# Kernel optimization log

Hardware: AMD Instinct MI355X
Metric: run time of the kernel (lower is better)

Reference implementation:

```python
import jax, jax.numpy as jnp
import numpy as np

B, T, D, H = 8, 1024, 512, 8
HD = D // H  # head_dim = 64


def conv1d(x, w, b):
    # x: [B, C_in, T], w: [C_out, C_in, 3], 'same' padding
    y = jax.lax.conv_general_dilated(x, w, (1,), [(1, 1)],
                                     dimension_numbers=('NCH', 'OIH', 'NCH'))
    return y + b[None, :, None]


def setup_inputs() -> dict:
    key = jax.random.key(0)
    ks = jax.random.split(key, 9)
    s = 0.05
    return {
        'x': jax.random.normal(ks[0], (B, T, D), dtype=jnp.float32),
        'w11': jax.random.normal(ks[1], (D, D, 3), dtype=jnp.float32) * s,
        'b11': jnp.zeros((D,), dtype=jnp.float32),
        'w12': jax.random.normal(ks[2], (D, D, 3), dtype=jnp.float32) * s,
        'b12': jnp.zeros((D,), dtype=jnp.float32),
        'w13': jax.random.normal(ks[3], (D, D, 3), dtype=jnp.float32) * s,
        'b13': jnp.zeros((D,), dtype=jnp.float32),
        'w2': jax.random.normal(ks[4], (D, 2 * D, 3), dtype=jnp.float32) * s,
        'b2': jnp.zeros((D,), dtype=jnp.float32),
    }


def reference(x, w11, b11, w12, b12, w13, b13, w2, b2):
    # dropout is identity in eval mode
    b, t, d = x.shape
    xc = jnp.transpose(x, (0, 2, 1))  # [B, D, T]

    def proj(w, bb):
        y = jax.nn.relu(conv1d(xc, w, bb))        # [B, D, T]
        y = jnp.transpose(y, (0, 2, 1))           # [B, T, D]
        return y.reshape(b, t, H, HD)             # [B, T, H, HD]

    q = proj(w11, b11)
    k = proj(w12, b12)
    v = proj(w13, b13)

    # ---- time-wise attention (d_k = head_dim) ----
    qf = jnp.transpose(q, (0, 2, 1, 3))  # [B, H, T, HD]
    kf = jnp.transpose(k, (0, 2, 1, 3))
    vf = jnp.transpose(v, (0, 2, 1, 3))
    sf = jnp.einsum('bhtd,bhsd->bhts', qf, kf) / np.sqrt(HD)  # [B,H,T,T]
    af = jax.nn.softmax(sf, axis=-1)
    valuesf = jnp.einsum('bhts,bhsd->bhtd', af, vf)           # [B,H,T,HD]
    valuesf = jnp.transpose(valuesf, (0, 2, 1, 3)).reshape(b, t, H * HD)

    # ---- channel-wise attention (d_k = T, scores over head_dim) ----
    qt = jnp.transpose(q, (0, 2, 3, 1))  # [B, H, HD, T]
    kt = jnp.transpose(k, (0, 2, 3, 1))
    vt = jnp.transpose(v, (0, 2, 3, 1))
    st = jnp.einsum('bhct,bhdt->bhcd', qt, kt) / np.sqrt(t)   # [B,H,HD,HD]
    at = jax.nn.softmax(st, axis=-1)
    valuest = jnp.einsum('bhcd,bhdt->bhct', at, vt)           # [B,H,HD,T]
    # torch: permute(0,2,3,1).reshape(B, T, H*HD)
    valuest = jnp.transpose(valuest, (0, 2, 3, 1)).reshape(b, t, H * HD)

    values = jnp.concatenate([valuesf, valuest], axis=-1)     # [B, T, 2D]
    values = jnp.transpose(values, (0, 2, 1))                 # [B, 2D, T]
    out = jax.nn.relu(conv1d(values, w2, b2))                 # [B, D, T]
    return jnp.transpose(out, (0, 2, 1))                      # [B, T, D]
```

## Files before the change

### kernel.cpp

```cpp
#include <hip/hip_runtime.h>

#define BB 8
#define TT 1024
#define DD 512
#define DD2 1024
#define HH 8
#define HDIM 64
#define TP (TT + 2)

typedef short short8 __attribute__((ext_vector_type(8)));
typedef float floatx4 __attribute__((ext_vector_type(4)));

typedef const __attribute__((address_space(1))) unsigned int* gas_ptr;
typedef __attribute__((address_space(3))) unsigned int* las_ptr;

__device__ __forceinline__ unsigned short f2bf(float f) {
    union { float f; unsigned u; } v; v.f = f;
    unsigned r = v.u + 0x7fffu + ((v.u >> 16) & 1u);
    return (unsigned short)(r >> 16);
}

__device__ __forceinline__ void gl2lds16(const void* g, void* l) {
    __builtin_amdgcn_global_load_lds((gas_ptr)g, (las_ptr)l, 16, 0, 0);
}

#define NX4BLK 4104
#define NW1BLK 9216
#define NW2BLK 6144
#define NZBLK 1024
__global__ void k_prep(const float* __restrict__ x, const float* __restrict__ w0,
                       const float* __restrict__ w1, const float* __restrict__ w2,
                       const float* __restrict__ wo,
                       unsigned short* __restrict__ xp, unsigned short* __restrict__ wqkv,
                       unsigned short* __restrict__ w2k, unsigned short* __restrict__ vp,
                       float* __restrict__ gbuf) {
    int blk = blockIdx.x;
    if (blk < NX4BLK) {
        int idx = blk * 256 + threadIdx.x;
        int c4 = idx % (DD / 4);
        int rt = idx / (DD / 4);
        int row = rt % TP;
        int b = rt / TP;
        ushort4 o = {0, 0, 0, 0};
        if (row >= 1 && row <= TT) {
            float4 vv = *(const float4*)&x[((size_t)(b * TT + row - 1)) * DD + c4 * 4];
            o.x = f2bf(vv.x); o.y = f2bf(vv.y); o.z = f2bf(vv.z); o.w = f2bf(vv.w);
        }
        *(ushort4*)&xp[(size_t)idx * 4] = o;
        return;
    }
    blk -= NX4BLK;
    if (blk < NW1BLK) {
        int idx = blk * 256 + threadIdx.x;
        int e = idx & 7;
        int lane = (idx >> 3) & 63;
        int co0 = (idx >> 9) & 31;
        int ci0 = (idx >> 14) & 15;
        int rest = idx >> 18;
        int k = rest % 3, p = rest / 3;
        int co = co0 * 16 + (lane & 15);
        int ci = ci0 * 32 + (lane >> 4) * 8 + e;
        const float* w = (p == 0) ? w0 : ((p == 1) ? w1 : w2);
        wqkv[idx] = f2bf(w[(co * DD + ci) * 3 + k]);
        return;
    }
    blk -= NW1BLK;
    if (blk < NW2BLK) {
        int idx = blk * 256 + threadIdx.x;
        int e = idx & 7;
        int lane = (idx >> 3) & 63;
        int co0 = (idx >> 9) & 31;
        int ci0 = (idx >> 14) & 31;
        int k = idx >> 19;
        int co = co0 * 16 + (lane & 15);
        int ci = ci0 * 32 + (lane >> 4) * 8 + e;
        w2k[idx] = f2bf(wo[(co * DD2 + ci) * 3 + k]);
        return;
    }
    blk -= NW2BLK;
    {
        int idx = blk * 256 + threadIdx.x;
        if (idx < BB * 2 * 2 * DD) {
            int c = idx % (2 * DD);
            int t1 = idx / (2 * DD);
            int row = (t1 & 1) ? (TT + 1) : 0;
            int b = t1 >> 1;
            vp[(b * TP + row) * (2 * DD) + c] = 0;
        }
        if (idx < 64 * HDIM * HDIM) gbuf[idx] = 0.f;
    }
}

__global__ __launch_bounds__(256) void k_qkv_conv(
    const unsigned short* __restrict__ xp, const unsigned short* __restrict__ wfrag,
    const float* __restrict__ b11, const float* __restrict__ b12, const float* __restrict__ b13,
    unsigned short* __restrict__ q, unsigned short* __restrict__ qt,
    unsigned short* __restrict__ kfrag, unsigned short* __restrict__ kt,
    unsigned short* __restrict__ v, unsigned short* __restrict__ vtfrag) {
    __shared__ short As[2][80 * 64];
    int wave = threadIdx.x >> 6, lane = threadIdx.x & 63;
    int l15 = lane & 15, quad = lane >> 4;
    int tb = blockIdx.x * 64;
    int cb = blockIdx.y * 128;
    int proj = blockIdx.z % 3, b = blockIdx.z / 3;
    const short* A = (const short*)xp + b * TP * DD;
    const short* WF = (const short*)wfrag + (size_t)proj * 786432 + lane * 8;
    int srow8 = lane >> 3;
    int scl = ((lane & 7) ^ srow8) * 8;
    int co0b = (cb >> 4) + wave * 2;

    floatx4 acc[4][2];
#pragma unroll
    for (int mi = 0; mi < 4; ++mi)
#pragma unroll
        for (int ni = 0; ni < 2; ++ni) acc[mi][ni] = (floatx4){0.f, 0.f, 0.f, 0.f};

    auto stage = [&](int it) {
        short* dst = As[it & 1];
        int cib = it * 64;
        for (int g = wave; g < 10; g += 4) {
            int j = g >> 1, hf = g & 1;
            int row = hf * 8 + srow8;
            gl2lds16(A + (tb + j * 16 + row) * DD + cib + scl, &dst[j * 1024 + hf * 512]);
        }
    };

    stage(0);
    __syncthreads();

    for (int it = 0; it < 8; ++it) {
        if (it < 7) stage(it + 1);
        const short* Asb = As[it & 1];
#pragma unroll
        for (int k = 0; k < 3; ++k) {
            short8 bf[2][2];
#pragma unroll
            for (int kf = 0; kf < 2; ++kf)
#pragma unroll
                for (int ni = 0; ni < 2; ++ni)
                    bf[kf][ni] = *(const short8*)(WF +
                        ((size_t)((k * 16 + it * 2 + kf) * 32 + co0b + ni) << 9));
#pragma unroll
            for (int kf = 0; kf < 2; ++kf) {
                short8 af[4];
#pragma unroll
                for (int mi = 0; mi < 4; ++mi) {
                    int arow = mi * 16 + l15 + k;
                    int cl = kf * 4 + quad;
                    af[mi] = *(const short8*)&Asb[arow * 64 + ((cl ^ (arow & 7)) << 3)];
                }
#pragma unroll
                for (int mi = 0; mi < 4; ++mi)
#pragma unroll
                    for (int ni = 0; ni < 2; ++ni)
                        acc[mi][ni] = __builtin_amdgcn_mfma_f32_16x16x32_bf16(af[mi], bf[kf][ni], acc[mi][ni], 0, 0, 0);
            }
        }
        __syncthreads();
    }

    const float* bias = (proj == 0) ? b11 : ((proj == 1) ? b12 : b13);
#pragma unroll
    for (int ni = 0; ni < 2; ++ni) {
        int co = cb + wave * 32 + ni * 16 + l15;
        float bv = bias[co];
        int h = co >> 6, hd = co & 63;
        int bh = b * HH + h;
#pragma unroll
        for (int mi = 0; mi < 4; ++mi) {
            int tbase = tb + mi * 16 + quad * 4;
            unsigned short bb[4];
            ushort4 pk;
#pragma unroll
            for (int r = 0; r < 4; ++r) {
                float val = fmaxf(acc[mi][ni][r] + bv, 0.f);
                bb[r] = f2bf(val);
                ((unsigned short*)&pk)[r] = bb[r];
            }
            if (proj == 0) {
#pragma unroll
                for (int r = 0; r < 4; ++r)
                    q[((size_t)bh * TT + tbase + r) * HDIM + hd] = bb[r];
                *(ushort4*)&qt[((size_t)bh * HDIM + hd) * TT + tbase] = pk;
            } else if (proj == 1) {
                *(ushort4*)&kt[((size_t)bh * HDIM + hd) * TT + tbase] = pk;
                int sblk = tbase >> 6;
                int jr = (quad & 1) + 2 * (mi >> 1);
                int l15a_base = 4 * (quad >> 1) + 8 * (mi & 1);
                int kf = hd >> 5, quad_a = (hd >> 3) & 3, elem = hd & 7;
                size_t base = ((((size_t)bh * 16 + sblk) * 4 + jr) * 2 + kf) * 512 +
                              quad_a * 128 + elem;
#pragma unroll
                for (int r = 0; r < 4; ++r)
                    kfrag[base + (l15a_base + r) * 8] = bb[r];
            } else {
#pragma unroll
                for (int r = 0; r < 4; ++r)
                    v[((size_t)bh * TT + tbase + r) * HDIM + hd] = bb[r];
                int sblk = tbase >> 6;
                int df = hd >> 4, l15a = hd & 15;
                int kf = mi >> 1;
                int quad_a = 2 * (mi & 1) + (quad >> 1);
                int elem = (quad & 1) * 4;
                size_t base = ((((size_t)bh * 16 + sblk) * 4 + df) * 2 + kf) * 512 +
                              (quad_a * 16 + l15a) * 8 + elem;
                *(ushort4*)&vtfrag[base] = pk;
            }
        }
    }
}

__global__ __launch_bounds__(256) void k_attn_gram(
    const unsigned short* __restrict__ q, const unsigned short* __restrict__ kfrag,
    const unsigned short* __restrict__ vtfrag, const unsigned short* __restrict__ qt,
    const unsigned short* __restrict__ kt, float* __restrict__ gbuf,
    unsigned short* __restrict__ vp) {
    __shared__ short kvs[2][8192];
    int wave = threadIdx.x >> 6, lane = threadIdx.x & 63;
    int l15 = lane & 15, quad = lane >> 4;
    int bh = blockIdx.y;

    if (blockIdx.x < 16) {
        int b = bh >> 3, h = bh & 7;
        int qr = blockIdx.x * 64 + wave * 16;
        const short* Q = (const short*)q + (size_t)bh * TT * HDIM;
        const short* KF = (const short*)kfrag + (size_t)bh * 16 * 8 * 512 + lane * 8;
        const short* VF = (const short*)vtfrag + (size_t)bh * 16 * 8 * 512 + lane * 8;

        short8 bq[2];
#pragma unroll
        for (int kf = 0; kf < 2; ++kf)
            bq[kf] = *(const short8*)(Q + (qr + l15) * HDIM + kf * 32 + quad * 8);

        floatx4 o[4];
#pragma unroll
        for (int df = 0; df < 4; ++df) o[df] = (floatx4){0.f, 0.f, 0.f, 0.f};
        float lacc = 0.f;

        auto stagekv = [&](int s) {
            short* dst = kvs[s & 1];
            for (int f = wave; f < 8; f += 4) {
                gl2lds16(KF + s * 4096 + f * 512, &dst[f * 512]);
                gl2lds16(VF + s * 4096 + f * 512, &dst[4096 + f * 512]);
            }
        };

        stagekv(0);
        __syncthreads();

        for (int sblk = 0; sblk < 16; ++sblk) {
            if (sblk < 15) stagekv(sblk + 1);
            const short* kb = (const short*)&kvs[sblk & 1][0] + lane * 8;
            const short* vb = kb + 4096;
            floatx4 c[4];
#pragma unroll
            for (int jr = 0; jr < 4; ++jr) c[jr] = (floatx4){0.f, 0.f, 0.f, 0.f};
#pragma unroll
            for (int jr = 0; jr < 4; ++jr) {
#pragma unroll
                for (int kf = 0; kf < 2; ++kf) {
                    short8 ak = *(const short8*)(kb + (jr * 2 + kf) * 512);
                    c[jr] = __builtin_amdgcn_mfma_f32_16x16x32_bf16(ak, bq[kf], c[jr], 0, 0, 0);
                }
            }
            short8 pb[2];
#pragma unroll
            for (int kf = 0; kf < 2; ++kf) {
                union { short8 s; unsigned u[4]; } pk;
#pragma unroll
                for (int half = 0; half < 2; ++half) {
                    floatx4 cc = c[2 * kf + half];
                    float p0 = __expf(cc[0] * 0.125f);
                    float p1 = __expf(cc[1] * 0.125f);
                    float p2 = __expf(cc[2] * 0.125f);
                    float p3 = __expf(cc[3] * 0.125f);
                    lacc += (p0 + p1) + (p2 + p3);
                    pk.u[half * 2] =
                        __builtin_amdgcn_perm(__float_as_uint(p1), __float_as_uint(p0), 0x07060302u);
                    pk.u[half * 2 + 1] =
                        __builtin_amdgcn_perm(__float_as_uint(p3), __float_as_uint(p2), 0x07060302u);
                }
                pb[kf] = pk.s;
            }
#pragma unroll
            for (int df = 0; df < 4; ++df) {
#pragma unroll
                for (int kf = 0; kf < 2; ++kf) {
                    short8 av = *(const short8*)(vb + (df * 2 + kf) * 512);
                    o[df] = __builtin_amdgcn_mfma_f32_16x16x32_bf16(av, pb[kf], o[df], 0, 0, 0);
                }
            }
            __syncthreads();
        }

        lacc += __shfl_xor(lacc, 16);
        lacc += __shfl_xor(lacc, 32);
        float linv = 1.f / lacc;

        unsigned short* vrow = vp + (size_t)(b * TP + 1 + qr + l15) * (2 * DD) + h * 64;
#pragma unroll
        for (int df = 0; df < 4; ++df) {
            ushort4 pk;
#pragma unroll
            for (int r = 0; r < 4; ++r) ((unsigned short*)&pk)[r] = f2bf(o[df][r] * linv);
            *(ushort4*)&vrow[df * 16 + quad * 4] = pk;
        }
    } else {
        int tc = blockIdx.x - 16;
        const short* Qt = (const short*)qt + (size_t)bh * HDIM * TT;
        const short* Kt = (const short*)kt + (size_t)bh * HDIM * TT;

        floatx4 g[4];
#pragma unroll
        for (int nt = 0; nt < 4; ++nt) g[nt] = (floatx4){0.f, 0.f, 0.f, 0.f};

        int t0b = tc * 256;
        for (int t0 = 0; t0 < 256; t0 += 32) {
            short8 aq = *(const short8*)(Qt + (wave * 16 + l15) * TT + t0b + t0 + quad * 8);
#pragma unroll
            for (int nt = 0; nt < 4; ++nt) {
                short8 bk = *(const short8*)(Kt + (nt * 16 + l15) * TT + t0b + t0 + quad * 8);
                g[nt] = __builtin_amdgcn_mfma_f32_16x16x32_bf16(aq, bk, g[nt], 0, 0, 0);
            }
        }
        float* gb = gbuf + bh * HDIM * HDIM;
#pragma unroll
        for (int nt = 0; nt < 4; ++nt) {
#pragma unroll
            for (int r = 0; r < 4; ++r) {
                int row = wave * 16 + quad * 4 + r;
                atomicAdd(&gb[row * HDIM + nt * 16 + l15], g[nt][r]);
            }
        }
    }
}

__global__ __launch_bounds__(256) void k_chan_av(
    const float* __restrict__ gbuf, const unsigned short* __restrict__ v,
    unsigned short* __restrict__ vp) {
    __shared__ short lds_a[64 * 64];
    int wave = threadIdx.x >> 6, lane = threadIdx.x & 63;
    int l15 = lane & 15, quad = lane >> 4;
    int tc = blockIdx.x, bh = blockIdx.y;
    int b = bh >> 3, h = bh & 7;
    const float sc = 0.03125f;

    if (threadIdx.x < 64) {
        const float* gb = gbuf + bh * HDIM * HDIM + threadIdx.x * HDIM;
        float mx = -3.0e38f;
        for (int j = 0; j < 64; ++j) mx = fmaxf(mx, gb[j] * sc);
        float sum = 0.f;
        for (int j = 0; j < 64; ++j) sum += __expf(gb[j] * sc - mx);
        float inv = 1.f / sum;
        for (int j = 0; j < 64; ++j)
            lds_a[threadIdx.x * 64 + j] = (short)f2bf(__expf(gb[j] * sc - mx) * inv);
    }
    __syncthreads();

    const short* V = (const short*)v + (size_t)bh * TT * HDIM;
    short8 pa[2];
#pragma unroll
    for (int kf = 0; kf < 2; ++kf)
        pa[kf] = *(const short8*)&lds_a[(wave * 16 + l15) * 64 + kf * 32 + quad * 8];

    for (int tt = 0; tt < 16; ++tt) {
        int ttile = tc * 16 + tt;
        floatx4 c = (floatx4){0.f, 0.f, 0.f, 0.f};
#pragma unroll
        for (int kf = 0; kf < 2; ++kf) {
            short8 bv = *(const short8*)(V + (ttile * 16 + l15) * HDIM + kf * 32 + quad * 8);
            c = __builtin_amdgcn_mfma_f32_16x16x32_bf16(pa[kf], bv, c, 0, 0, 0);
        }
        int t = ttile * 16 + l15;
#pragma unroll
        for (int r = 0; r < 4; ++r) {
            int crow = wave * 16 + quad * 4 + r;
            int tout = crow * 16 + (t >> 6);
            int col = 512 + ((t & 63) << 3) + h;
            vp[(b * TP + 1 + tout) * (2 * DD) + col] = f2bf(c[r]);
        }
    }
}

__global__ __launch_bounds__(256) void k_out_conv(
    const unsigned short* __restrict__ vp, const unsigned short* __restrict__ w2k,
    const float* __restrict__ b2, float* __restrict__ out) {
    __shared__ short As[2][144 * 64];
    int wave = threadIdx.x >> 6, lane = threadIdx.x & 63;
    int l15 = lane & 15, quad = lane >> 4;
    int wm = wave >> 1, wn = wave & 1;
    int tb = blockIdx.x * 128;
    int cb = blockIdx.y * 64;
    int b = blockIdx.z;
    const short* A = (const short*)vp + b * TP * DD2;
    const short* WF = (const short*)w2k + lane * 8;
    int srow8 = lane >> 3;
    int scl = ((lane & 7) ^ srow8) * 8;
    int co0b = (cb >> 4) + wn * 2;

    floatx4 acc[4][2];
#pragma unroll
    for (int mi = 0; mi < 4; ++mi)
#pragma unroll
        for (int ni = 0; ni < 2; ++ni) acc[mi][ni] = (floatx4){0.f, 0.f, 0.f, 0.f};

    auto stage = [&](int it) {
        short* dst = As[it & 1];
        int cib = it * 64;
        for (int g = wave; g < 18; g += 4) {
            int j = g >> 1, hf = g & 1;
            int row = hf * 8 + srow8;
            gl2lds16(A + (tb + j * 16 + row) * DD2 + cib + scl, &dst[j * 1024 + hf * 512]);
        }
    };

    stage(0);
    __syncthreads();

    for (int it = 0; it < 16; ++it) {
        if (it < 15) stage(it + 1);
        const short* Asb = As[it & 1];
#pragma unroll
        for (int k = 0; k < 3; ++k) {
            short8 bf[2][2];
#pragma unroll
            for (int kfh = 0; kfh < 2; ++kfh)
#pragma unroll
                for (int ni = 0; ni < 2; ++ni)
                    bf[kfh][ni] = *(const short8*)(WF +
                        ((size_t)((k * 32 + it * 2 + kfh) * 32 + co0b + ni) << 9));
#pragma unroll
            for (int kfh = 0; kfh < 2; ++kfh) {
                short8 af[4];
#pragma unroll
                for (int mi = 0; mi < 4; ++mi) {
                    int arow = wm * 64 + mi * 16 + l15 + k;
                    int cl = kfh * 4 + quad;
                    af[mi] = *(const short8*)&Asb[arow * 64 + ((cl ^ (arow & 7)) << 3)];
                }
#pragma unroll
                for (int mi = 0; mi < 4; ++mi)
#pragma unroll
                    for (int ni = 0; ni < 2; ++ni)
                        acc[mi][ni] = __builtin_amdgcn_mfma_f32_16x16x32_bf16(af[mi], bf[kfh][ni], acc[mi][ni], 0, 0, 0);
            }
        }
        __syncthreads();
    }

#pragma unroll
    for (int ni = 0; ni < 2; ++ni) {
        int co = cb + wn * 32 + ni * 16 + l15;
        float bv = b2[co];
#pragma unroll
        for (int mi = 0; mi < 4; ++mi) {
#pragma unroll
            for (int r = 0; r < 4; ++r) {
                int t = tb + wm * 64 + mi * 16 + quad * 4 + r;
                out[((size_t)b * TT + t) * DD + co] = fmaxf(acc[mi][ni][r] + bv, 0.f);
            }
        }
    }
}

extern "C" void kernel_launch(void* const* d_in, const int* in_sizes, int n_in,
                              void* d_out, int out_size, void* d_ws, size_t ws_size,
                              hipStream_t stream) {
    const float* x = (const float*)d_in[0];
    const float* w11 = (const float*)d_in[1];
    const float* b11 = (const float*)d_in[2];
    const float* w12 = (const float*)d_in[3];
    const float* b12 = (const float*)d_in[4];
    const float* w13 = (const float*)d_in[5];
    const float* b13 = (const float*)d_in[6];
    const float* w2 = (const float*)d_in[7];
    const float* b2 = (const float*)d_in[8];
    float* out = (float*)d_out;

    char* ws = (char*)d_ws;
    size_t off = 0;
    auto alloc = [&](size_t bytes) {
        void* p = ws + off;
        off += (bytes + 255) & ~(size_t)255;
        return p;
    };
    unsigned short* xp = (unsigned short*)alloc((size_t)BB * TP * DD * 2);
    unsigned short* wqkv = (unsigned short*)alloc((size_t)9 * DD * DD * 2);
    unsigned short* w2k = (unsigned short*)alloc((size_t)3 * DD * DD2 * 2);
    unsigned short* q = (unsigned short*)alloc((size_t)BB * HH * TT * HDIM * 2);
    unsigned short* qt = (unsigned short*)alloc((size_t)BB * HH * TT * HDIM * 2);
    unsigned short* kfrag = (unsigned short*)alloc((size_t)BB * HH * TT * HDIM * 2);
    unsigned short* kt = (unsigned short*)alloc((size_t)BB * HH * TT * HDIM * 2);
    unsigned short* v = (unsigned short*)alloc((size_t)BB * HH * TT * HDIM * 2);
    unsigned short* vtfrag = (unsigned short*)alloc((size_t)BB * HH * TT * HDIM * 2);
    float* gbuf = (float*)alloc((size_t)64 * HDIM * HDIM * 4);
    unsigned short* vp = (unsigned short*)alloc((size_t)BB * TP * 2 * DD * 2);
    (void)alloc(65536);

    k_prep<<<NX4BLK + NW1BLK + NW2BLK + NZBLK, 256, 0, stream>>>(x, w11, w12, w13, w2,
                                                                 xp, wqkv, w2k, vp, gbuf);
    k_qkv_conv<<<dim3(TT / 64, DD / 128, BB * 3), 256, 0, stream>>>(xp, wqkv, b11, b12, b13,
                                                                    q, qt, kfrag, kt, v, vtfrag);
    k_attn_gram<<<dim3(20, BB * HH), 256, 0, stream>>>(q, kfrag, vtfrag, qt, kt, gbuf, vp);
    k_chan_av<<<dim3(4, BB * HH), 256, 0, stream>>>(gbuf, v, vp);
    k_out_conv<<<dim3(TT / 128, DD / 64, BB), 256, 0, stream>>>(vp, w2k, b2, out);
}
```

Baseline: 218.2 us.

## Hoist weight fragment loads and use vmcnt-based barriers in conv kernels; drop q buffer

In both conv GEMM kernels, all weight fragments for an iteration are loaded up front. The full __syncthreads is replaced with a partial s_waitcnt vmcnt plus s_barrier, so the async LDS stage for the next tile can stay in flight while the current tile is consumed. The separate q output buffer is also removed, and the attention kernel gathers its Q fragments from the transposed qt with strided scalar loads. This saves a scattered store pass but makes the Q load in attention uncoalesced. The hand-counted vmcnt values are fragile if the compiler changes how many loads it issues.

Result: slower. 222.9 us (+2.1%).

```diff
diff --git a/kernel.cpp b/kernel.cpp
--- a/kernel.cpp
+++ b/kernel.cpp
@@ -94,7 +94,7 @@
 __global__ __launch_bounds__(256) void k_qkv_conv(
     const unsigned short* __restrict__ xp, const unsigned short* __restrict__ wfrag,
     const float* __restrict__ b11, const float* __restrict__ b12, const float* __restrict__ b13,
-    unsigned short* __restrict__ q, unsigned short* __restrict__ qt,
+    unsigned short* __restrict__ qt,
     unsigned short* __restrict__ kfrag, unsigned short* __restrict__ kt,
     unsigned short* __restrict__ v, unsigned short* __restrict__ vtfrag) {
     __shared__ short As[2][80 * 64];
@@ -126,20 +126,30 @@
     };
 
     stage(0);
-    __syncthreads();
 
     for (int it = 0; it < 8; ++it) {
+        short8 bf[3][2][2];
+#pragma unroll
+        for (int k = 0; k < 3; ++k)
+#pragma unroll
+            for (int kf = 0; kf < 2; ++kf)
+#pragma unroll
+                for (int ni = 0; ni < 2; ++ni)
+                    bf[k][kf][ni] = *(const short8*)(WF +
+                        ((size_t)((k * 16 + it * 2 + kf) * 32 + co0b + ni) << 9));
+        __builtin_amdgcn_sched_barrier(0);
         if (it < 7) stage(it + 1);
+        if (it < 7) {
+            if (wave < 2) asm volatile("s_waitcnt vmcnt(15)" ::: "memory");
+            else          asm volatile("s_waitcnt vmcnt(14)" ::: "memory");
+        } else {
+            asm volatile("s_waitcnt vmcnt(12)" ::: "memory");
+        }
+        __builtin_amdgcn_s_barrier();
+        __builtin_amdgcn_sched_barrier(0);
         const short* Asb = As[it & 1];
 #pragma unroll
         for (int k = 0; k < 3; ++k) {
-            short8 bf[2][2];
-#pragma unroll
-            for (int kf = 0; kf < 2; ++kf)
-#pragma unroll
-                for (int ni = 0; ni < 2; ++ni)
-                    bf[kf][ni] = *(const short8*)(WF +
-                        ((size_t)((k * 16 + it * 2 + kf) * 32 + co0b + ni) << 9));
 #pragma unroll
             for (int kf = 0; kf < 2; ++kf) {
                 short8 af[4];
@@ -153,10 +163,10 @@
                 for (int mi = 0; mi < 4; ++mi)
 #pragma unroll
                     for (int ni = 0; ni < 2; ++ni)
-                        acc[mi][ni] = __builtin_amdgcn_mfma_f32_16x16x32_bf16(af[mi], bf[kf][ni], acc[mi][ni], 0, 0, 0);
-            }
-        }
-        __syncthreads();
+                        acc[mi][ni] = __builtin_amdgcn_mfma_f32_16x16x32_bf16(af[mi], bf[k][kf][ni], acc[mi][ni], 0, 0, 0);
+            }
+        }
+        __builtin_amdgcn_s_barrier();
     }
 
     const float* bias = (proj == 0) ? b11 : ((proj == 1) ? b12 : b13);
@@ -178,9 +188,6 @@
                 ((unsigned short*)&pk)[r] = bb[r];
             }
             if (proj == 0) {
-#pragma unroll
-                for (int r = 0; r < 4; ++r)
-                    q[((size_t)bh * TT + tbase + r) * HDIM + hd] = bb[r];
                 *(ushort4*)&qt[((size_t)bh * HDIM + hd) * TT + tbase] = pk;
             } else if (proj == 1) {
                 *(ushort4*)&kt[((size_t)bh * HDIM + hd) * TT + tbase] = pk;
@@ -211,10 +218,9 @@
 }
 
 __global__ __launch_bounds__(256) void k_attn_gram(
-    const unsigned short* __restrict__ q, const unsigned short* __restrict__ kfrag,
-    const unsigned short* __restrict__ vtfrag, const unsigned short* __restrict__ qt,
-    const unsigned short* __restrict__ kt, float* __restrict__ gbuf,
-    unsigned short* __restrict__ vp) {
+    const unsigned short* __restrict__ kfrag, const unsigned short* __restrict__ vtfrag,
+    const unsigned short* __restrict__ qt, const unsigned short* __restrict__ kt,
+    float* __restrict__ gbuf, unsigned short* __restrict__ vp) {
     __shared__ short kvs[2][8192];
     int wave = threadIdx.x >> 6, lane = threadIdx.x & 63;
     int l15 = lane & 15, quad = lane >> 4;
@@ -223,14 +229,19 @@
     if (blockIdx.x < 16) {
         int b = bh >> 3, h = bh & 7;
         int qr = blockIdx.x * 64 + wave * 16;
-        const short* Q = (const short*)q + (size_t)bh * TT * HDIM;
+        const short* Qt = (const short*)qt + (size_t)bh * HDIM * TT;
         const short* KF = (const short*)kfrag + (size_t)bh * 16 * 8 * 512 + lane * 8;
         const short* VF = (const short*)vtfrag + (size_t)bh * 16 * 8 * 512 + lane * 8;
 
         short8 bq[2];
 #pragma unroll
-        for (int kf = 0; kf < 2; ++kf)
-            bq[kf] = *(const short8*)(Q + (qr + l15) * HDIM + kf * 32 + quad * 8);
+        for (int kf = 0; kf < 2; ++kf) {
+            union { short8 s; short v[8]; } u;
+#pragma unroll
+            for (int e = 0; e < 8; ++e)
+                u.v[e] = Qt[(size_t)(kf * 32 + quad * 8 + e) * TT + qr + l15];
+            bq[kf] = u.s;
+        }
 
         floatx4 o[4];
 #pragma unroll
@@ -415,20 +426,30 @@
     };
 
     stage(0);
-    __syncthreads();
 
     for (int it = 0; it < 16; ++it) {
+        short8 bf[3][2][2];
+#pragma unroll
+        for (int k = 0; k < 3; ++k)
+#pragma unroll
+            for (int kfh = 0; kfh < 2; ++kfh)
+#pragma unroll
+                for (int ni = 0; ni < 2; ++ni)
+                    bf[k][kfh][ni] = *(const short8*)(WF +
+                        ((size_t)((k * 32 + it * 2 + kfh) * 32 + co0b + ni) << 9));
+        __builtin_amdgcn_sched_barrier(0);
         if (it < 15) stage(it + 1);
+        if (it < 15) {
+            if (wave < 2) asm volatile("s_waitcnt vmcnt(17)" ::: "memory");
+            else          asm volatile("s_waitcnt vmcnt(16)" ::: "memory");
+        } else {
+            asm volatile("s_waitcnt vmcnt(12)" ::: "memory");
+        }
+        __builtin_amdgcn_s_barrier();
+        __builtin_amdgcn_sched_barrier(0);
         const short* Asb = As[it & 1];
 #pragma unroll
         for (int k = 0; k < 3; ++k) {
-            short8 bf[2][2];
-#pragma unroll
-            for (int kfh = 0; kfh < 2; ++kfh)
-#pragma unroll
-                for (int ni = 0; ni < 2; ++ni)
-                    bf[kfh][ni] = *(const short8*)(WF +
-                        ((size_t)((k * 32 + it * 2 + kfh) * 32 + co0b + ni) << 9));
 #pragma unroll
             for (int kfh = 0; kfh < 2; ++kfh) {
                 short8 af[4];
@@ -442,10 +463,10 @@
                 for (int mi = 0; mi < 4; ++mi)
 #pragma unroll
                     for (int ni = 0; ni < 2; ++ni)
-                        acc[mi][ni] = __builtin_amdgcn_mfma_f32_16x16x32_bf16(af[mi], bf[kfh][ni], acc[mi][ni], 0, 0, 0);
-            }
-        }
-        __syncthreads();
+                        acc[mi][ni] = __builtin_amdgcn_mfma_f32_16x16x32_bf16(af[mi], bf[k][kfh][ni], acc[mi][ni], 0, 0, 0);
+            }
+        }
+        __builtin_amdgcn_s_barrier();
     }
 
 #pragma unroll
@@ -487,7 +508,6 @@
     unsigned short* xp = (unsigned short*)alloc((size_t)BB * TP * DD * 2);
     unsigned short* wqkv = (unsigned short*)alloc((size_t)9 * DD * DD * 2);
     unsigned short* w2k = (unsigned short*)alloc((size_t)3 * DD * DD2 * 2);
-    unsigned short* q = (unsigned short*)alloc((size_t)BB * HH * TT * HDIM * 2);
     unsigned short* qt = (unsigned short*)alloc((size_t)BB * HH * TT * HDIM * 2);
     unsigned short* kfrag = (unsigned short*)alloc((size_t)BB * HH * TT * HDIM * 2);
     unsigned short* kt = (unsigned short*)alloc((size_t)BB * HH * TT * HDIM * 2);
@@ -500,8 +520,8 @@
     k_prep<<<NX4BLK + NW1BLK + NW2BLK + NZBLK, 256, 0, stream>>>(x, w11, w12, w13, w2,
                                                                  xp, wqkv, w2k, vp, gbuf);
     k_qkv_conv<<<dim3(TT / 64, DD / 128, BB * 3), 256, 0, stream>>>(xp, wqkv, b11, b12, b13,
-                                                                    q, qt, kfrag, kt, v, vtfrag);
-    k_attn_gram<<<dim3(20, BB * HH), 256, 0, stream>>>(q, kfrag, vtfrag, qt, kt, gbuf, vp);
+                                                                    qt, kfrag, kt, v, vtfrag);
+    k_attn_gram<<<dim3(20, BB * HH), 256, 0, stream>>>(kfrag, vtfrag, qt, kt, gbuf, vp);
     k_chan_av<<<dim3(4, BB * HH), 256, 0, stream>>>(gbuf, v, vp);
     k_out_conv<<<dim3(TT / 128, DD / 64, BB), 256, 0, stream>>>(vp, w2k, b2, out);
 }
```

## Compute Q, K, V projections in one block reusing staged input tile

Applied to the files above, without the earlier changes.

The QKV convolution kernel now loads the full 80x512 input tile for a batch/time block into shared memory once and loops over the three projections inside the block, instead of launching a separate block per projection that restages the same input. The separate row-major q buffer is dropped, and the attention kernel gathers its Q fragments from the transposed qt buffer with strided scalar loads. Shared memory per block grows to about 80 KB and the grid shrinks threefold, which lowers occupancy and removes the old double-buffered load/compute overlap. The Q fragment loads are now uncoalesced.

Result: slower. 488.5 us (+123.9%).

```diff
diff --git a/kernel.cpp b/kernel.cpp
--- a/kernel.cpp
+++ b/kernel.cpp
@@ -94,127 +94,121 @@
 __global__ __launch_bounds__(256) void k_qkv_conv(
     const unsigned short* __restrict__ xp, const unsigned short* __restrict__ wfrag,
     const float* __restrict__ b11, const float* __restrict__ b12, const float* __restrict__ b13,
-    unsigned short* __restrict__ q, unsigned short* __restrict__ qt,
+    unsigned short* __restrict__ qt,
     unsigned short* __restrict__ kfrag, unsigned short* __restrict__ kt,
     unsigned short* __restrict__ v, unsigned short* __restrict__ vtfrag) {
-    __shared__ short As[2][80 * 64];
+    __shared__ short As[8][80 * 64];
     int wave = threadIdx.x >> 6, lane = threadIdx.x & 63;
     int l15 = lane & 15, quad = lane >> 4;
     int tb = blockIdx.x * 64;
     int cb = blockIdx.y * 128;
-    int proj = blockIdx.z % 3, b = blockIdx.z / 3;
+    int b = blockIdx.z;
     const short* A = (const short*)xp + b * TP * DD;
-    const short* WF = (const short*)wfrag + (size_t)proj * 786432 + lane * 8;
     int srow8 = lane >> 3;
     int scl = ((lane & 7) ^ srow8) * 8;
     int co0b = (cb >> 4) + wave * 2;
 
-    floatx4 acc[4][2];
-#pragma unroll
-    for (int mi = 0; mi < 4; ++mi)
-#pragma unroll
-        for (int ni = 0; ni < 2; ++ni) acc[mi][ni] = (floatx4){0.f, 0.f, 0.f, 0.f};
-
-    auto stage = [&](int it) {
-        short* dst = As[it & 1];
+    for (int it = 0; it < 8; ++it) {
+        short* dst = As[it];
         int cib = it * 64;
         for (int g = wave; g < 10; g += 4) {
             int j = g >> 1, hf = g & 1;
             int row = hf * 8 + srow8;
             gl2lds16(A + (tb + j * 16 + row) * DD + cib + scl, &dst[j * 1024 + hf * 512]);
         }
-    };
-
-    stage(0);
+    }
     __syncthreads();
 
-    for (int it = 0; it < 8; ++it) {
-        if (it < 7) stage(it + 1);
-        const short* Asb = As[it & 1];
-#pragma unroll
-        for (int k = 0; k < 3; ++k) {
-            short8 bf[2][2];
-#pragma unroll
-            for (int kf = 0; kf < 2; ++kf)
-#pragma unroll
-                for (int ni = 0; ni < 2; ++ni)
-                    bf[kf][ni] = *(const short8*)(WF +
-                        ((size_t)((k * 16 + it * 2 + kf) * 32 + co0b + ni) << 9));
-#pragma unroll
-            for (int kf = 0; kf < 2; ++kf) {
-                short8 af[4];
-#pragma unroll
-                for (int mi = 0; mi < 4; ++mi) {
-                    int arow = mi * 16 + l15 + k;
-                    int cl = kf * 4 + quad;
-                    af[mi] = *(const short8*)&Asb[arow * 64 + ((cl ^ (arow & 7)) << 3)];
-                }
-#pragma unroll
-                for (int mi = 0; mi < 4; ++mi)
+    for (int proj = 0; proj < 3; ++proj) {
+        const short* WF = (const short*)wfrag + (size_t)proj * 786432 + lane * 8;
+        floatx4 acc[4][2];
+#pragma unroll
+        for (int mi = 0; mi < 4; ++mi)
+#pragma unroll
+            for (int ni = 0; ni < 2; ++ni) acc[mi][ni] = (floatx4){0.f, 0.f, 0.f, 0.f};
+
+        for (int it = 0; it < 8; ++it) {
+            const short* Asb = As[it];
+#pragma unroll
+            for (int k = 0; k < 3; ++k) {
+                short8 bf[2][2];
+#pragma unroll
+                for (int kf = 0; kf < 2; ++kf)
 #pragma unroll
                     for (int ni = 0; ni < 2; ++ni)
-                        acc[mi][ni] = __builtin_amdgcn_mfma_f32_16x16x32_bf16(af[mi], bf[kf][ni], acc[mi][ni], 0, 0, 0);
-            }
-        }
-        __syncthreads();
-    }
-
-    const float* bias = (proj == 0) ? b11 : ((proj == 1) ? b12 : b13);
-#pragma unroll
-    for (int ni = 0; ni < 2; ++ni) {
-        int co = cb + wave * 32 + ni * 16 + l15;
-        float bv = bias[co];
-        int h = co >> 6, hd = co & 63;
-        int bh = b * HH + h;
-#pragma unroll
-        for (int mi = 0; mi < 4; ++mi) {
-            int tbase = tb + mi * 16 + quad * 4;
-            unsigned short bb[4];
-            ushort4 pk;
-#pragma unroll
-            for (int r = 0; r < 4; ++r) {
-                float val = fmaxf(acc[mi][ni][r] + bv, 0.f);
-                bb[r] = f2bf(val);
-                ((unsigned short*)&pk)[r] = bb[r];
-            }
-            if (proj == 0) {
-#pragma unroll
-                for (int r = 0; r < 4; ++r)
-                    q[((size_t)bh * TT + tbase + r) * HDIM + hd] = bb[r];
-                *(ushort4*)&qt[((size_t)bh * HDIM + hd) * TT + tbase] = pk;
-            } else if (proj == 1) {
-                *(ushort4*)&kt[((size_t)bh * HDIM + hd) * TT + tbase] = pk;
-                int sblk = tbase >> 6;
-                int jr = (quad & 1) + 2 * (mi >> 1);
-                int l15a_base = 4 * (quad >> 1) + 8 * (mi & 1);
-                int kf = hd >> 5, quad_a = (hd >> 3) & 3, elem = hd & 7;
-                size_t base = ((((size_t)bh * 16 + sblk) * 4 + jr) * 2 + kf) * 512 +
-                              quad_a * 128 + elem;
-#pragma unroll
-                for (int r = 0; r < 4; ++r)
-                    kfrag[base + (l15a_base + r) * 8] = bb[r];
-            } else {
-#pragma unroll
-                for (int r = 0; r < 4; ++r)
-                    v[((size_t)bh * TT + tbase + r) * HDIM + hd] = bb[r];
-                int sblk = tbase >> 6;
-                int df = hd >> 4, l15a = hd & 15;
-                int kf = mi >> 1;
-                int quad_a = 2 * (mi & 1) + (quad >> 1);
-                int elem = (quad & 1) * 4;
-                size_t base = ((((size_t)bh * 16 + sblk) * 4 + df) * 2 + kf) * 512 +
-                              (quad_a * 16 + l15a) * 8 + elem;
-                *(ushort4*)&vtfrag[base] = pk;
+                        bf[kf][ni] = *(const short8*)(WF +
+                            ((size_t)((k * 16 + it * 2 + kf) * 32 + co0b + ni) << 9));
+#pragma unroll
+                for (int kf = 0; kf < 2; ++kf) {
+                    short8 af[4];
+#pragma unroll
+                    for (int mi = 0; mi < 4; ++mi) {
+                        int arow = mi * 16 + l15 + k;
+                        int cl = kf * 4 + quad;
+                        af[mi] = *(const short8*)&Asb[arow * 64 + ((cl ^ (arow & 7)) << 3)];
+                    }
+#pragma unroll
+                    for (int mi = 0; mi < 4; ++mi)
+#pragma unroll
+                        for (int ni = 0; ni < 2; ++ni)
+                            acc[mi][ni] = __builtin_amdgcn_mfma_f32_16x16x32_bf16(af[mi], bf[kf][ni], acc[mi][ni], 0, 0, 0);
+                }
+            }
+        }
+
+        const float* bias = (proj == 0) ? b11 : ((proj == 1) ? b12 : b13);
+#pragma unroll
+        for (int ni = 0; ni < 2; ++ni) {
+            int co = cb + wave * 32 + ni * 16 + l15;
+            float bv = bias[co];
+            int h = co >> 6, hd = co & 63;
+            int bh = b * HH + h;
+#pragma unroll
+            for (int mi = 0; mi < 4; ++mi) {
+                int tbase = tb + mi * 16 + quad * 4;
+                unsigned short bb[4];
+                ushort4 pk;
+#pragma unroll
+                for (int r = 0; r < 4; ++r) {
+                    float val = fmaxf(acc[mi][ni][r] + bv, 0.f);
+                    bb[r] = f2bf(val);
+                    ((unsigned short*)&pk)[r] = bb[r];
+                }
+                if (proj == 0) {
+                    *(ushort4*)&qt[((size_t)bh * HDIM + hd) * TT + tbase] = pk;
+                } else if (proj == 1) {
+                    *(ushort4*)&kt[((size_t)bh * HDIM + hd) * TT + tbase] = pk;
+                    int sblk = tbase >> 6;
+                    int jr = (quad & 1) + 2 * (mi >> 1);
+                    int l15a_base = 4 * (quad >> 1) + 8 * (mi & 1);
+                    int kf = hd >> 5, quad_a = (hd >> 3) & 3, elem = hd & 7;
+                    size_t base = ((((size_t)bh * 16 + sblk) * 4 + jr) * 2 + kf) * 512 +
+                                  quad_a * 128 + elem;
+#pragma unroll
+                    for (int r = 0; r < 4; ++r)
+                        kfrag[base + (l15a_base + r) * 8] = bb[r];
+                } else {
+#pragma unroll
+                    for (int r = 0; r < 4; ++r)
+                        v[((size_t)bh * TT + tbase + r) * HDIM + hd] = bb[r];
+                    int sblk = tbase >> 6;
+                    int df = hd >> 4, l15a = hd & 15;
+                    int kf = mi >> 1;
+                    int quad_a = 2 * (mi & 1) + (quad >> 1);
+                    int elem = (quad & 1) * 4;
+                    size_t base = ((((size_t)bh * 16 + sblk) * 4 + df) * 2 + kf) * 512 +
+                                  (quad_a * 16 + l15a) * 8 + elem;
+                    *(ushort4*)&vtfrag[base] = pk;
+                }
             }
         }
     }
 }
 
 __global__ __launch_bounds__(256) void k_attn_gram(
-    const unsigned short* __restrict__ q, const unsigned short* __restrict__ kfrag,
-    const unsigned short* __restrict__ vtfrag, const unsigned short* __restrict__ qt,
-    const unsigned short* __restrict__ kt, float* __restrict__ gbuf,
-    unsigned short* __restrict__ vp) {
+    const unsigned short* __restrict__ kfrag, const unsigned short* __restrict__ vtfrag,
+    const unsigned short* __restrict__ qt, const unsigned short* __restrict__ kt,
+    float* __restrict__ gbuf, unsigned short* __restrict__ vp) {
     __shared__ short kvs[2][8192];
     int wave = threadIdx.x >> 6, lane = threadIdx.x & 63;
     int l15 = lane & 15, quad = lane >> 4;
@@ -223,14 +217,19 @@
     if (blockIdx.x < 16) {
         int b = bh >> 3, h = bh & 7;
         int qr = blockIdx.x * 64 + wave * 16;
-        const short* Q = (const short*)q + (size_t)bh * TT * HDIM;
+        const short* Qt = (const short*)qt + (size_t)bh * HDIM * TT;
         const short* KF = (const short*)kfrag + (size_t)bh * 16 * 8 * 512 + lane * 8;
         const short* VF = (const short*)vtfrag + (size_t)bh * 16 * 8 * 512 + lane * 8;
 
         short8 bq[2];
 #pragma unroll
-        for (int kf = 0; kf < 2; ++kf)
-            bq[kf] = *(const short8*)(Q + (qr + l15) * HDIM + kf * 32 + quad * 8);
+        for (int kf = 0; kf < 2; ++kf) {
+            union { short8 s; short v[8]; } u;
+#pragma unroll
+            for (int e = 0; e < 8; ++e)
+                u.v[e] = Qt[(size_t)(kf * 32 + quad * 8 + e) * TT + qr + l15];
+            bq[kf] = u.s;
+        }
 
         floatx4 o[4];
 #pragma unroll
@@ -487,7 +486,6 @@
     unsigned short* xp = (unsigned short*)alloc((size_t)BB * TP * DD * 2);
     unsigned short* wqkv = (unsigned short*)alloc((size_t)9 * DD * DD * 2);
     unsigned short* w2k = (unsigned short*)alloc((size_t)3 * DD * DD2 * 2);
-    unsigned short* q = (unsigned short*)alloc((size_t)BB * HH * TT * HDIM * 2);
     unsigned short* qt = (unsigned short*)alloc((size_t)BB * HH * TT * HDIM * 2);
     unsigned short* kfrag = (unsigned short*)alloc((size_t)BB * HH * TT * HDIM * 2);
     unsigned short* kt = (unsigned short*)alloc((size_t)BB * HH * TT * HDIM * 2);
@@ -499,9 +497,9 @@
 
     k_prep<<<NX4BLK + NW1BLK + NW2BLK + NZBLK, 256, 0, stream>>>(x, w11, w12, w13, w2,
                                                                  xp, wqkv, w2k, vp, gbuf);
-    k_qkv_conv<<<dim3(TT / 64, DD / 128, BB * 3), 256, 0, stream>>>(xp, wqkv, b11, b12, b13,
-                                                                    q, qt, kfrag, kt, v, vtfrag);
-    k_attn_gram<<<dim3(20, BB * HH), 256, 0, stream>>>(q, kfrag, vtfrag, qt, kt, gbuf, vp);
+    k_qkv_conv<<<dim3(TT / 64, DD / 128, BB), 256, 0, stream>>>(xp, wqkv, b11, b12, b13,
+                                                                qt, kfrag, kt, v, vtfrag);
+    k_attn_gram<<<dim3(20, BB * HH), 256, 0, stream>>>(kfrag, vtfrag, qt, kt, gbuf, vp);
     k_chan_av<<<dim3(4, BB * HH), 256, 0, stream>>>(gbuf, v, vp);
     k_out_conv<<<dim3(TT / 128, DD / 64, BB), 256, 0, stream>>>(vp, w2k, b2, out);
 }
```
